# Optimization experiments

Hardware: AMD Instinct MI355X
Metric: run time of the kernel (lower is better)

The kernel has to match this reference:

```python
import jax, jax.numpy as jnp
import numpy as np

B, F, D, K = 4096, 1, 256, 65536

def setup_inputs() -> dict:
    key = jax.random.key(0)
    k1, k2, k3 = jax.random.split(key, 3)
    xhat_BFD = jax.random.normal(k1, (B, F, D), dtype=jnp.float32)
    x_BD = jax.random.normal(k2, (B * F, D), dtype=jnp.float32)
    centroids = jax.random.normal(k3, (K, D), dtype=jnp.float32)
    return {"xhat_BFD": xhat_BFD, "x_BD": x_BD, "centroids": centroids}

def reference(xhat_BFD, x_BD, centroids):
    c_sq_K = jnp.sum(centroids * centroids, axis=-1)            # [K]
    dists_BK = c_sq_K[None, :] - 2.0 * (x_BD @ centroids.T)     # [B*F, K] (GEMM-based distances)
    codes_B = jnp.argmin(dists_BK, axis=-1)                      # [B*F]
    quant_x_BD = centroids[codes_B]                              # embedding lookup of winners
    Bb, Ff, Dd = xhat_BFD.shape
    xhat_next = quant_x_BD.reshape(Bb, Ff, Dd)
    codes_BF = codes_B.reshape(Bb, Ff)
    return xhat_next, codes_BF
```

## Files before the change

kernel.cpp:

```cpp
#include <hip/hip_runtime.h>
#include <hip/hip_bf16.h>
#include <math.h>


#define DDIM 256
#define QTILE 128
#define STSZ 8192
#define QCAP 48
#define F16_MINN 6.103515625e-5f

typedef __attribute__((ext_vector_type(8))) _Float16 half8;
typedef __attribute__((ext_vector_type(4))) _Float16 half4;
typedef __attribute__((ext_vector_type(4))) float f32x4;
typedef __attribute__((ext_vector_type(16))) float f32x16;

__device__ __forceinline__ void gl_lds16(const void* g, void* l) {
  __builtin_amdgcn_global_load_lds((const __attribute__((address_space(1))) void*)g,
                                   (__attribute__((address_space(3))) void*)l, 16, 0, 0);
}

__device__ __forceinline__ unsigned fkey(float d) {
  unsigned ud = __float_as_uint(d);
  return ud ^ (((int)ud < 0) ? 0xFFFFFFFFu : 0x80000000u);
}

__global__ void initctl_kernel(unsigned* __restrict__ ctl) {
  if (threadIdx.x < 64) ctl[threadIdx.x] = 0u;
}

__global__ __launch_bounds__(256) void splitc_kernel(const float* __restrict__ in,
                                                     _Float16* __restrict__ o0,
                                                     float* __restrict__ c_sq) {
  int i = blockIdx.x * 256 + threadIdx.x;
  int lane = (int)threadIdx.x & 63;
  float4 v = ((const float4*)in)[i];
  float vv[4] = {v.x, v.y, v.z, v.w};
  half4 h0;
#pragma unroll
  for (int e = 0; e < 4; ++e)
    h0[e] = (fabsf(vv[e]) < F16_MINN) ? (_Float16)0.f : (_Float16)vv[e];
  *(half4*)(o0 + (size_t)i * 4) = h0;
  float s = fmaf(v.x, v.x, fmaf(v.y, v.y, fmaf(v.z, v.z, v.w * v.w)));
#pragma unroll
  for (int off = 32; off > 0; off >>= 1) s += __shfl_down(s, off, 64);
  if (lane == 0) c_sq[i >> 6] = s;
}

__global__ __launch_bounds__(256) void splitx_kernel(const float* __restrict__ in,
                                                     _Float16* __restrict__ o0, int n4) {
  int i = blockIdx.x * 256 + threadIdx.x;
  if (i >= n4) return;
  float4 v = ((const float4*)in)[i];
  float vv[4] = {v.x, v.y, v.z, v.w};
  half4 h0;
#pragma unroll
  for (int e = 0; e < 4; ++e)
    h0[e] = (fabsf(vv[e]) < F16_MINN) ? (_Float16)0.f : (_Float16)vv[e];
  *(half4*)(o0 + (size_t)i * 4) = h0;
}

__global__ __launch_bounds__(256) void cmax_kernel(const float* __restrict__ c_sq,
                                                   unsigned* __restrict__ ctl) {
  __shared__ float red[4];
  int t = blockIdx.x * 256 + (int)threadIdx.x;
  float4 v = ((const float4*)c_sq)[t];
  float m = fmaxf(fmaxf(v.x, v.y), fmaxf(v.z, v.w));
#pragma unroll
  for (int off = 32; off > 0; off >>= 1) m = fmaxf(m, __shfl_down(m, off, 64));
  int lane = (int)threadIdx.x & 63, w = (int)threadIdx.x >> 6;
  if (lane == 0) red[w] = m;
  __syncthreads();
  if (threadIdx.x == 0) {
    m = fmaxf(fmaxf(red[0], red[1]), fmaxf(red[2], red[3]));
    atomicMax(&ctl[32], __float_as_uint(m));
  }
}

__global__ __launch_bounds__(1024) void scan_kernel(
    const _Float16* __restrict__ x0, const _Float16* __restrict__ c0,
    const float* __restrict__ c_sq, float* __restrict__ dm) {
  __shared__ __align__(16) _Float16 As0[32768];

  const int qb = blockIdx.x, kc = blockIdx.y;
  const int tid = (int)threadIdx.x;
  const int lane = tid & 63, w = tid >> 6;
  const int lo = lane & 31, hi = lane >> 5;
  const int qrow0 = qb * QTILE;

#pragma unroll
  for (int i = 0; i < 4; ++i) {
    int u = i * 1024 + tid;
    int q = u & 127, s = u >> 7;
    gl_lds16(x0 + (size_t)(qrow0 + q) * DDIM + s * 8, As0 + (size_t)u * 8);
  }
  __syncthreads();

  for (int ct = 0; ct < STSZ / 512; ++ct) {
    const int cbase = kc * STSZ + ct * 512 + w * 32;
    f32x16 acc[4];
#pragma unroll
    for (int qn = 0; qn < 4; ++qn) acc[qn] = (f32x16)0.0f;

#pragma unroll 4
    for (int kt = 0; kt < 16; ++kt) {
      half8 cf = *(const half8*)(c0 + (size_t)(cbase + lo) * DDIM + kt * 16 + hi * 8);
#pragma unroll
      for (int qn = 0; qn < 4; ++qn) {
        half8 qf = *(const half8*)(As0 + (size_t)(((kt * 2 + hi) * QTILE) + qn * 32 + lo) * 8);
        acc[qn] = __builtin_amdgcn_mfma_f32_32x32x16_f16(cf, qf, acc[qn], 0, 0, 0);
      }
    }

    f32x4 csv[4];
#pragma unroll
    for (int g = 0; g < 4; ++g)
      csv[g] = *(const f32x4*)(c_sq + cbase + g * 8 + hi * 4);
    const int grp = kc * (STSZ / 32) + ct * 16 + w;
    float* dmg = dm + (size_t)grp * 4096 + qrow0;
#pragma unroll
    for (int qn = 0; qn < 4; ++qn) {
      float mq = INFINITY;
#pragma unroll
      for (int r = 0; r < 16; ++r)
        mq = fminf(mq, fmaf(-2.0f, acc[qn][r], csv[r >> 2][r & 3]));
      mq = fminf(mq, __shfl_xor(mq, 32, 64));
      if (hi == 0) dmg[qn * 32 + lo] = mq;
    }
  }
}

__global__ __launch_bounds__(256) void pmin_kernel(const float* __restrict__ dm,
                                                   float* __restrict__ pm) {
  int qc = blockIdx.x & 15, gc = blockIdx.x >> 4;
  int q = qc * 256 + (int)threadIdx.x;
  float m = INFINITY;
  for (int g = gc * 128; g < gc * 128 + 128; ++g)
    m = fminf(m, dm[(size_t)g * 4096 + q]);
  pm[gc * 4096 + q] = m;
}

__global__ __launch_bounds__(256) void tq_kernel(const float* __restrict__ pm,
                                                 const float* __restrict__ x,
                                                 const unsigned* __restrict__ ctl,
                                                 float* __restrict__ T,
                                                 unsigned* __restrict__ cnt) {
  int q = blockIdx.x * 256 + (int)threadIdx.x;
  float M = INFINITY;
#pragma unroll
  for (int i = 0; i < 16; ++i) M = fminf(M, pm[i * 4096 + q]);
  float xsq = 0.f;
  const float4* xr = (const float4*)(x + (size_t)q * DDIM);
#pragma unroll 8
  for (int i = 0; i < 64; ++i) {
    float4 v = xr[i];
    xsq = fmaf(v.x, v.x, fmaf(v.y, v.y, fmaf(v.z, v.z, fmaf(v.w, v.w, xsq))));
  }
  float cmaxsq = __uint_as_float(ctl[32]);
  T[q] = M + 0.0078125f * sqrtf(xsq * cmaxsq) + 1.0f;
  cnt[q] = 0u;
}

__global__ __launch_bounds__(256) void emit_kernel(const float* __restrict__ dm,
                                                   const float* __restrict__ T,
                                                   unsigned short* __restrict__ cand,
                                                   unsigned* __restrict__ cnt) {
  int qc = blockIdx.x & 15, gc = blockIdx.x >> 4;
  int q = qc * 256 + (int)threadIdx.x;
  float t = T[q];
  for (int g = gc * 128; g < gc * 128 + 128; ++g)
    if (dm[(size_t)g * 4096 + q] <= t) {
      unsigned slot = atomicAdd(&cnt[q], 1u);
      if (slot < QCAP) cand[(size_t)q * QCAP + slot] = (unsigned short)g;
    }
}

__global__ __launch_bounds__(256) void rescore_final_kernel(
    const unsigned short* __restrict__ cand, const unsigned* __restrict__ cnt,
    const float* __restrict__ x, const float* __restrict__ cent,
    const float* __restrict__ c_sq, float* __restrict__ out) {
  int q = blockIdx.x * 4 + ((int)threadIdx.x >> 6);
  int lane = (int)threadIdx.x & 63;
  unsigned n = cnt[q];
  unsigned long long best = 0xFFFFFFFFFFFFFFFFull;
  if (n >= 1 && n <= QCAP) {
    int dh = (lane & 1) * 128;
    const float4* xr = (const float4*)(x + (size_t)q * DDIM + dh);
    for (unsigned sl = 0; sl < n; ++sl) {
      int g = (int)cand[(size_t)q * QCAP + sl];
      int c = g * 32 + (lane >> 1);
      const float4* cr = (const float4*)(cent + (size_t)c * DDIM + dh);
      float s = 0.f;
#pragma unroll
      for (int i = 0; i < 32; ++i) {
        float4 a = xr[i], bb = cr[i];
        s = fmaf(a.x, bb.x, fmaf(a.y, bb.y, fmaf(a.z, bb.z, fmaf(a.w, bb.w, s))));
      }
      s += __shfl_xor(s, 1, 64);
      float d = (lane & 1) ? INFINITY : fmaf(-2.0f, s, c_sq[c]);
      unsigned long long pkv = ((unsigned long long)fkey(d) << 32) | (unsigned)c;
      if (pkv < best) best = pkv;
    }
  } else {
    const float4* xr = (const float4*)(x + (size_t)q * DDIM);
    for (int c = lane; c < 65536; c += 64) {
      const float4* cr = (const float4*)(cent + (size_t)c * DDIM);
      float s = 0.f;
#pragma unroll 16
      for (int i = 0; i < 64; ++i) {
        float4 a = xr[i], bb = cr[i];
        s = fmaf(a.x, bb.x, fmaf(a.y, bb.y, fmaf(a.z, bb.z, fmaf(a.w, bb.w, s))));
      }
      float d = fmaf(-2.0f, s, c_sq[c]);
      unsigned long long pkv = ((unsigned long long)fkey(d) << 32) | (unsigned)c;
      if (pkv < best) best = pkv;
    }
  }
#pragma unroll
  for (int off = 1; off < 64; off <<= 1) {
    unsigned long long o = __shfl_xor(best, off, 64);
    if (o < best) best = o;
  }
  int idx = (int)(unsigned)(best & 0xFFFFFFFFu);
  float4 v = ((const float4*)cent)[(size_t)idx * 64 + lane];
  ((float4*)out)[(size_t)q * 64 + lane] = v;
  if (lane == 0) out[(size_t)4096 * DDIM + q] = (float)idx;
}

extern "C" void kernel_launch(void* const* d_in, const int* in_sizes, int n_in,
                              void* d_out, int out_size, void* d_ws, size_t ws_size,
                              hipStream_t stream) {
  const float* x    = (const float*)d_in[1];
  const float* cent = (const float*)d_in[2];
  float* out = (float*)d_out;
  char* ws = (char*)d_ws;

  const size_t OFF_C0   = 0;
  const size_t OFF_X0   = 33554432;
  const size_t OFF_CSQ  = 35651584;
  const size_t OFF_CTL  = 35913728;
  const size_t OFF_DM   = 35913984;
  const size_t OFF_PM   = 69468416;
  const size_t OFF_T    = 69730560;
  const size_t OFF_CNT  = 69746944;
  const size_t OFF_CAND = 69763328;
  const size_t NEED     = 72089600;
  if (ws_size < NEED) return;

  _Float16* c0 = (_Float16*)(ws + OFF_C0);
  _Float16* x0 = (_Float16*)(ws + OFF_X0);
  float* c_sq = (float*)(ws + OFF_CSQ);
  unsigned* ctl = (unsigned*)(ws + OFF_CTL);
  float* dm = (float*)(ws + OFF_DM);
  float* pm = (float*)(ws + OFF_PM);
  float* T  = (float*)(ws + OFF_T);
  unsigned* cnt = (unsigned*)(ws + OFF_CNT);
  unsigned short* cand = (unsigned short*)(ws + OFF_CAND);

  initctl_kernel<<<1, 64, 0, stream>>>(ctl);
  splitc_kernel<<<16384, 256, 0, stream>>>(cent, c0, c_sq);
  splitx_kernel<<<1024, 256, 0, stream>>>(x, x0, 4096 * 256 / 4);
  cmax_kernel<<<64, 256, 0, stream>>>(c_sq, ctl);
  scan_kernel<<<dim3(32, 8), 1024, 0, stream>>>(x0, c0, c_sq, dm);
  pmin_kernel<<<256, 256, 0, stream>>>(dm, pm);
  tq_kernel<<<16, 256, 0, stream>>>(pm, x, ctl, T, cnt);
  emit_kernel<<<256, 256, 0, stream>>>(dm, T, cand, cnt);
  rescore_final_kernel<<<1024, 256, 0, stream>>>(cand, cnt, x, cent, c_sq, out);
}
```

Before: 401.5 us.

## Double-buffer centroid tiles through LDS with async global-to-LDS loads in scan

```diff
diff --git a/kernel.cpp b/kernel.cpp
--- a/kernel.cpp
+++ b/kernel.cpp
@@ -80,12 +80,14 @@
     const _Float16* __restrict__ x0, const _Float16* __restrict__ c0,
     const float* __restrict__ c_sq, float* __restrict__ dm) {
   __shared__ __align__(16) _Float16 As0[32768];
-
-  const int qb = blockIdx.x, kc = blockIdx.y;
+  __shared__ __align__(16) _Float16 Cs[2][16384];
+
+  const int kc = blockIdx.x, qb = blockIdx.y;
   const int tid = (int)threadIdx.x;
   const int lane = tid & 63, w = tid >> 6;
   const int lo = lane & 31, hi = lane >> 5;
   const int qrow0 = qb * QTILE;
+  const size_t cstrip = (size_t)kc * STSZ;
 
 #pragma unroll
   for (int i = 0; i < 4; ++i) {
@@ -93,6 +95,12 @@
     int q = u & 127, s = u >> 7;
     gl_lds16(x0 + (size_t)(qrow0 + q) * DDIM + s * 8, As0 + (size_t)u * 8);
   }
+#pragma unroll
+  for (int i = 0; i < 2; ++i) {
+    int u2 = i * 1024 + tid;
+    int s = u2 >> 9, c = u2 & 511;
+    gl_lds16(c0 + (cstrip + c) * DDIM + s * 8, Cs[0] + (size_t)u2 * 8);
+  }
   __syncthreads();
 
   for (int ct = 0; ct < STSZ / 512; ++ct) {
@@ -101,14 +109,31 @@
 #pragma unroll
     for (int qn = 0; qn < 4; ++qn) acc[qn] = (f32x16)0.0f;
 
-#pragma unroll 4
-    for (int kt = 0; kt < 16; ++kt) {
-      half8 cf = *(const half8*)(c0 + (size_t)(cbase + lo) * DDIM + kt * 16 + hi * 8);
-#pragma unroll
-      for (int qn = 0; qn < 4; ++qn) {
-        half8 qf = *(const half8*)(As0 + (size_t)(((kt * 2 + hi) * QTILE) + qn * 32 + lo) * 8);
-        acc[qn] = __builtin_amdgcn_mfma_f32_32x32x16_f16(cf, qf, acc[qn], 0, 0, 0);
-      }
+#pragma unroll
+    for (int ktp = 0; ktp < 8; ++ktp) {
+      const int cur = ktp & 1;
+      if (ct * 8 + ktp + 1 < 128) {
+        const int nu = ct * 8 + ktp + 1;
+        const int nct = nu >> 3, nktp = nu & 7;
+#pragma unroll
+        for (int i = 0; i < 2; ++i) {
+          int u2 = i * 1024 + tid;
+          int s = u2 >> 9, c = u2 & 511;
+          gl_lds16(c0 + (cstrip + (size_t)nct * 512 + c) * DDIM + nktp * 32 + s * 8,
+                   Cs[cur ^ 1] + (size_t)u2 * 8);
+        }
+      }
+#pragma unroll
+      for (int kt2 = 0; kt2 < 2; ++kt2) {
+        const int kt = ktp * 2 + kt2;
+        half8 cf = *(const half8*)(Cs[cur] + ((size_t)(kt2 * 2 + hi) * 512 + w * 32 + lo) * 8);
+#pragma unroll
+        for (int qn = 0; qn < 4; ++qn) {
+          half8 qf = *(const half8*)(As0 + (size_t)(((kt * 2 + hi) * QTILE) + qn * 32 + lo) * 8);
+          acc[qn] = __builtin_amdgcn_mfma_f32_32x32x16_f16(cf, qf, acc[qn], 0, 0, 0);
+        }
+      }
+      __syncthreads();
     }
 
     f32x4 csv[4];
@@ -260,7 +285,7 @@
   splitc_kernel<<<16384, 256, 0, stream>>>(cent, c0, c_sq);
   splitx_kernel<<<1024, 256, 0, stream>>>(x, x0, 4096 * 256 / 4);
   cmax_kernel<<<64, 256, 0, stream>>>(c_sq, ctl);
-  scan_kernel<<<dim3(32, 8), 1024, 0, stream>>>(x0, c0, c_sq, dm);
+  scan_kernel<<<dim3(8, 32), 1024, 0, stream>>>(x0, c0, c_sq, dm);
   pmin_kernel<<<256, 256, 0, stream>>>(dm, pm);
   tq_kernel<<<16, 256, 0, stream>>>(pm, x, ctl, T, cnt);
   emit_kernel<<<256, 256, 0, stream>>>(dm, T, cand, cnt);
```

After: 498.5 us. 24.2% more time.
